# Optimization experiments

Measured on AMD Instinct MI355X. Metric: run time of the kernel, lower is better.

Reference implementation:

```python
import jax, jax.numpy as jnp
from jax import lax
import numpy as np

T_STEPS, C_IN, H_IN, W_IN = 15, 6, 256, 256
C_OUT, KSIZE = 64, 5
THRESH = 15.0   # conv_t[0]
KWTA = 5        # ks[0]
INH_R = 3       # inh_radiuses[0]


def setup_inputs() -> dict:
    key = jax.random.key(0)
    k1, k2 = jax.random.split(key)
    # cumulative binary spike-wave: once a unit spikes it stays on (SpykeTorch convention)
    bern = jax.random.uniform(k1, (T_STEPS, C_IN, H_IN, W_IN)) < 0.05
    spikes = (jnp.cumsum(bern.astype(jnp.int32), axis=0) > 0).astype(jnp.float32)
    # SpykeTorch Convolution init: N(0.8, 0.05)
    w1 = 0.8 + 0.05 * jax.random.normal(k2, (C_OUT, C_IN, KSIZE, KSIZE), dtype=jnp.float32)
    return {"input": spikes, "w1": w1, "current_layer_id": 1}


def pointwise_inhibition(thr_pot):
    # thr_pot: (T, C, H, W). Keep, at each spatial position, only the feature
    # with the earliest spike (ties broken by max potential); zero the rest.
    T = thr_pot.shape[0]
    C = thr_pot.shape[1]
    max_vals = jnp.max(thr_pot, axis=1, keepdims=True)            # (T,1,H,W)
    max_idx = jnp.argmax(thr_pot, axis=1, keepdims=True)          # (T,1,H,W)
    clamp_pot = jnp.sign(max_vals)                                # (T,1,H,W) in {0,1}
    earliest = jnp.clip((T - clamp_pot.sum(axis=0, keepdims=True)).astype(jnp.int32), 0, T - 1)  # (1,1,H,W)
    winners = jnp.take_along_axis(max_idx, earliest, axis=0)      # (1,1,H,W)
    onehot = (jnp.arange(C)[None, :, None, None] == winners[:, 0])  # (1,C,H,W)
    coef = onehot.astype(thr_pot.dtype) * clamp_pot[-1:]          # zero where no spike at last step
    return thr_pot * coef


def get_k_winners(pot, spk, kwta, inh_radius):
    # pot, spk: (T, C, H, W). Returns (kwta, 3) int winners (c, h, w); -1 rows = no winner.
    T, C, H, W = pot.shape
    earliest = jnp.clip((T - spk.sum(axis=0, keepdims=True)).astype(jnp.int32), 0, T - 1)
    values = jnp.take_along_axis(pot, earliest, axis=0)           # (1,C,H,W)
    trunc = spk * values
    v = trunc.max() * T
    trunc = trunc + spk * v
    total = trunc.sum(axis=0)                                     # (C,H,W)
    rows = jnp.arange(H)
    cols = jnp.arange(W)

    def step(total, _):
        idx = jnp.argmax(total)
        val = total.reshape(-1)[idx]
        c = idx // (H * W)
        rem = idx % (H * W)
        h = rem // W
        w = rem % W
        winner = jnp.where(val != 0,
                           jnp.stack([c, h, w]),
                           jnp.full((3,), -1, dtype=idx.dtype))
        total = total.at[c].set(0.0)
        box = (((rows >= h - inh_radius) & (rows <= h + inh_radius))[:, None]
               & ((cols >= w - inh_radius) & (cols <= w + inh_radius))[None, :])
        total = jnp.where(box[None, :, :], 0.0, total)            # columnar spatial inhibition
        return total, winner

    _, winners = lax.scan(step, total, None, length=kwta)
    return winners


def reference(input, w1, current_layer_id):
    # training path, current_layer_id == 1
    x = jnp.pad(input.astype(jnp.float32), ((0, 0), (0, 0), (2, 2), (2, 2)))  # sf.pad (2,2,2,2)
    pot = lax.conv_general_dilated(x, w1, (1, 1), 'VALID',
                                   dimension_numbers=('NCHW', 'OIHW', 'NCHW'))  # (T,64,256,256)
    pot = jnp.where(pot < THRESH, 0.0, pot)   # sf.fire -> thresholded potentials
    pot = pointwise_inhibition(pot)
    spk = jnp.sign(pot)
    winners = get_k_winners(pot, spk, KWTA, INH_R)
    return spk, pot, winners
```

## Files before the change

### kernel.cpp

```cpp
#include <hip/hip_runtime.h>
#include <hip/hip_cooperative_groups.h>
#include <stdint.h>

namespace cg = cooperative_groups;

static constexpr int T_STEPS = 15;
static constexpr int C_IN = 6;
static constexpr int C_OUT = 64;
static constexpr int H = 256;
static constexpr int W = 256;
static constexpr int NPOS = H * W;
static constexpr int NTAP = 150;
#define DTHRESH 15.0

typedef float vfloat4 __attribute__((ext_vector_type(4)));

static constexpr size_t WS_FT     = 0;
static constexpr size_t WS_SERIES = 393216;
static constexpr size_t WS_WINC   = WS_SERIES + (size_t)NPOS*16*4;
static constexpr size_t WS_NMAP   = WS_WINC + (size_t)NPOS;
static constexpr size_t WS_VAL    = WS_NMAP + (size_t)NPOS;
static constexpr size_t WS_RED    = WS_VAL + (size_t)NPOS*8;
static constexpr size_t WS_RIX    = WS_RED + 128*8;
static constexpr size_t WS_NEED   = WS_RIX + 128*4;

__global__ __launch_bounds__(256) void ft_kernel(const float* __restrict__ x,
                                                 uint8_t* __restrict__ ft) {
    int i = blockIdx.x * 256 + threadIdx.x;
    if (i >= C_IN * NPOS) return;
    int f = 15;
    #pragma unroll
    for (int t = T_STEPS - 1; t >= 0; --t) {
        if (x[(size_t)t * (C_IN * NPOS) + i] > 0.0f) f = t;
    }
    ft[i] = (uint8_t)f;
}

__global__ __launch_bounds__(256, 4) void conv_kernel(
        const float* __restrict__ w1, const uint8_t* __restrict__ ftg,
        float* __restrict__ series_ws, int8_t* __restrict__ winc_ws,
        uint8_t* __restrict__ nmap_ws, double* __restrict__ val_ws)
{
    __shared__ float w_lds[(NTAP + 1) * 64];
    __shared__ uint8_t ft_lds[6 * 5 * 20];
    __shared__ alignas(16) unsigned cnt_lds[4][16];
    __shared__ alignas(8) uint8_t sorted_lds[4][200];

    int tid = threadIdx.x;
    int bid = blockIdx.x;
    int h  = bid >> 4;
    int w0 = (bid & 15) << 4;

    for (int i = tid; i < C_OUT * NTAP; i += 256) {
        int o = i / NTAP;
        int tap = i - o * NTAP;
        w_lds[tap * 64 + o] = w1[i];
    }
    if (tid < 64) w_lds[NTAP * 64 + tid] = 0.0f;
    for (int i = tid; i < 600; i += 256) {
        int c = i / 100;
        int r = i - c * 100;
        int kh = r / 20;
        int j  = r - kh * 20;
        int gh = h - 2 + kh;
        int gw = w0 - 2 + j;
        uint8_t v = 15;
        if (gh >= 0 && gh < H && gw >= 0 && gw < W) v = ftg[c * NPOS + gh * W + gw];
        ft_lds[(c * 5 + kh) * 20 + j] = v;
    }
    __syncthreads();

    int lane = tid & 63;
    int wvi  = tid >> 6;
    unsigned* cnt = cnt_lds[wvi];
    uint8_t* srt = sorted_lds[wvi];

    for (int iter = 0; iter < 4; ++iter) {
        int xl = iter * 4 + wvi;
        int p  = h * W + w0 + xl;

        if (lane < 16) cnt[lane] = 0;

        int tap0 = lane, tap1 = lane + 64, tap2 = lane + 128;
        auto ftv = [&](int tap) -> unsigned {
            int c = tap / 25;
            int r = tap - c * 25;
            int kh = r / 5;
            int kw = r - kh * 5;
            return ft_lds[(c * 5 + kh) * 20 + xl + kw];
        };
        unsigned f0 = ftv(tap0);
        unsigned f1 = ftv(tap1);
        unsigned f2 = (tap2 < NTAP) ? ftv(tap2) : 15u;
        unsigned r0 = 0, r1 = 0, r2 = 0;
        if (f0 < 15u) r0 = atomicAdd(&cnt[f0], 1u);
        if (f1 < 15u) r1 = atomicAdd(&cnt[f1], 1u);
        if (f2 < 15u) r2 = atomicAdd(&cnt[f2], 1u);

        uint4 c4[4];
        #pragma unroll
        for (int i = 0; i < 4; ++i) c4[i] = ((const uint4*)cnt)[i];
        unsigned cv_t[16];
        #pragma unroll
        for (int i = 0; i < 4; ++i) {
            cv_t[4*i+0] = c4[i].x; cv_t[4*i+1] = c4[i].y;
            cv_t[4*i+2] = c4[i].z; cv_t[4*i+3] = c4[i].w;
        }
        int kt[15];
        #pragma unroll
        for (int t = 0; t < 15; ++t) kt[t] = (int)__builtin_amdgcn_readfirstlane(cv_t[t]);

        unsigned st0 = 0, st1 = 0, st2 = 0, stp = 0;
        #pragma unroll
        for (int t = 0; t < 15; ++t) {
            unsigned a = (cv_t[t] + 3u) & ~3u;
            if ((unsigned)t < f0) st0 += a;
            if ((unsigned)t < f1) st1 += a;
            if ((unsigned)t < f2) st2 += a;
            if (t < lane) stp += a;
        }
        if (f0 < 15u) srt[st0 + r0] = (uint8_t)tap0;
        if (f1 < 15u) srt[st1 + r1] = (uint8_t)tap1;
        if (f2 < 15u) srt[st2 + r2] = (uint8_t)tap2;

        if (lane < 15) {
            unsigned kk = cnt[lane];
            unsigned a4 = (kk + 3u) & ~3u;
            if (kk     < a4) srt[stp + kk]     = (uint8_t)NTAP;
            if (kk + 1 < a4) srt[stp + kk + 1] = (uint8_t)NTAP;
            if (kk + 2 < a4) srt[stp + kk + 2] = (uint8_t)NTAP;
        }

        double run = 0.0, cvv = 0.0;
        int tc = 127;
        float ser[15];
        int A = 0;
        #pragma unroll
        for (int t = 0; t < 15; ++t) {
            int k = kt[t];
            for (int q = 0; q < k; q += 4) {
                unsigned pr = *(const unsigned*)(srt + A + q);
                float wa  = w_lds[((pr       & 0xFFu) << 6) + lane];
                float wb  = w_lds[(((pr >> 8) & 0xFFu) << 6) + lane];
                float wcf = w_lds[(((pr >> 16) & 0xFFu) << 6) + lane];
                float wd  = w_lds[(( pr >> 24        ) << 6) + lane];
                float s   = (wa + wb) + (wcf + wd);
                run += (double)s;
            }
            A += (k + 3) & ~3;
            ser[t] = (float)run;
            bool cross_now = (tc == 127) && (run >= DTHRESH);
            if (cross_now) { tc = t; cvv = run; }
        }

        int e = tc;
        #pragma unroll
        for (int off = 32; off >= 1; off >>= 1) e = min(e, __shfl_xor(e, off));
        int wc = -1;
        double val = 0.0;
        if (e < 15) {
            double vl = (tc == e) ? cvv : 0.0;
            double m = vl;
            #pragma unroll
            for (int off = 32; off >= 1; off >>= 1) m = fmax(m, __shfl_xor(m, off));
            unsigned long long mk = __ballot(vl == m);
            wc = __ffsll(mk) - 1;
            val = m;

            float ov = 0.0f;
            #pragma unroll
            for (int t = 0; t < 15; ++t) {
                float sv = __shfl(ser[t], wc);
                if (lane == t) ov = sv;
            }
            if (lane < e) ov = 0.0f;
            if (lane < 15) series_ws[p * 16 + lane] = ov;
        }
        if (lane == 0) {
            winc_ws[p] = (int8_t)wc;
            nmap_ws[p] = (uint8_t)(wc >= 0 ? (15 - e) : 0);
            if (wc >= 0) val_ws[p] = val;
        }
    }
}

__global__ __launch_bounds__(256) void kwin_kernel(
        const int8_t* __restrict__ winc, const uint8_t* __restrict__ nmap,
        const double* __restrict__ val, float* __restrict__ outw,
        double* __restrict__ redv, unsigned* __restrict__ redi)
{
    cg::grid_group grid = cg::this_grid();
    const int tid  = threadIdx.x;
    const int bid  = blockIdx.x;
    const int lane = tid & 63, wvi = tid >> 6;

    __shared__ double   s_v[4];
    __shared__ unsigned s_i[4];

    int     pc[4];
    int     phh[4], pww[4];
    double  key[4];
    unsigned idx[4];
    bool    alive[4];
    #pragma unroll
    for (int k = 0; k < 4; ++k) {
        const int p = (k << 14) | (bid << 8) | tid;
        const int c = winc[p];
        alive[k] = (c >= 0);
        const double vp = alive[k] ? val[p] : 0.0;
        key[k]  = (double)nmap[p] * 2048.0 + vp;
        idx[k]  = ((unsigned)c << 16) | (unsigned)p;
        pc[k]   = c;
        phh[k]  = p >> 8;
        pww[k]  = p & 255;
    }

    for (int r = 0; r < 5; ++r) {
        __syncthreads();
        const int par = r & 1;

        double   bv = -1.0;
        unsigned bi = 0xFFFFFFFFu;
        #pragma unroll
        for (int k = 0; k < 4; ++k) {
            if (alive[k] && (key[k] > bv || (key[k] == bv && idx[k] < bi))) {
                bv = key[k]; bi = idx[k];
            }
        }
        #pragma unroll
        for (int off = 32; off >= 1; off >>= 1) {
            double   ov = __shfl_xor(bv, off);
            unsigned oi = __shfl_xor(bi, off);
            if (ov > bv || (ov == bv && oi < bi)) { bv = ov; bi = oi; }
        }
        if (lane == 0) { s_v[wvi] = bv; s_i[wvi] = bi; }
        __syncthreads();
        if (tid == 0) {
            double bbv = s_v[0]; unsigned bbi = s_i[0];
            #pragma unroll
            for (int i = 1; i < 4; ++i)
                if (s_v[i] > bbv || (s_v[i] == bbv && s_i[i] < bbi)) { bbv = s_v[i]; bbi = s_i[i]; }
            redv[par * 64 + bid] = bbv;
            redi[par * 64 + bid] = bbi;
        }
        grid.sync();

        if (wvi == 0) {
            double   gv = redv[par * 64 + lane];
            unsigned gi = redi[par * 64 + lane];
            #pragma unroll
            for (int off = 32; off >= 1; off >>= 1) {
                double   ov = __shfl_xor(gv, off);
                unsigned oi = __shfl_xor(gi, off);
                if (ov > gv || (ov == gv && oi < gi)) { gv = ov; gi = oi; }
            }
            if (lane == 0) { s_v[0] = gv; s_i[0] = gi; }
        }
        __syncthreads();
        const double   bbv = s_v[0];
        const unsigned bbi = s_i[0];

        const bool valid = (bbv > 0.0);
        if (bid == 0 && tid == 0) {
            int wc2 = (int)(bbi >> 16), pp = (int)(bbi & 0xFFFFu);
            outw[r * 3 + 0] = valid ? (float)wc2       : -1.0f;
            outw[r * 3 + 1] = valid ? (float)(pp >> 8) : -1.0f;
            outw[r * 3 + 2] = valid ? (float)(pp & 255): -1.0f;
        }
        if (valid) {
            const int wc2 = (int)(bbi >> 16);
            const int wp  = (int)(bbi & 0xFFFFu);
            const int wh  = wp >> 8, wwv = wp & 255;
            #pragma unroll
            for (int k = 0; k < 4; ++k) {
                if (pc[k] == wc2 || (phh[k] >= wh - 3 && phh[k] <= wh + 3 &&
                                     pww[k] >= wwv - 3 && pww[k] <= wwv + 3)) alive[k] = false;
            }
        }
    }
}

__global__ __launch_bounds__(256) void expand_kernel(
        const int8_t* __restrict__ winc, const float* __restrict__ series,
        float* __restrict__ spk, float* __restrict__ pot)
{
    int idx4 = blockIdx.x * 256 + threadIdx.x;
    int w4 = idx4 & 63;
    int h  = (idx4 >> 6) & 255;
    int c  = (idx4 >> 14) & 63;
    int t  = idx4 >> 20;
    int pbase = h * W + (w4 << 2);
    uint32_t wcs = *reinterpret_cast<const uint32_t*>(winc + pbase);
    vfloat4 pv = (vfloat4)(0.0f);
    vfloat4 sv = (vfloat4)(0.0f);
    #pragma unroll
    for (int e2 = 0; e2 < 4; ++e2) {
        int8_t wcb = (int8_t)((wcs >> (8 * e2)) & 0xFFu);
        if ((int)wcb == c) {
            float xv = series[(size_t)(pbase + e2) * 16 + t];
            pv[e2] = xv;
            sv[e2] = (xv > 0.f) ? 1.0f : 0.0f;
        }
    }
    reinterpret_cast<vfloat4*>(spk)[idx4] = sv;
    reinterpret_cast<vfloat4*>(pot)[idx4] = pv;
}

extern "C" void kernel_launch(void* const* d_in, const int* in_sizes, int n_in,
                              void* d_out, int out_size, void* d_ws, size_t ws_size,
                              hipStream_t stream)
{
    if (ws_size < WS_NEED) return;

    const float* x  = (const float*)d_in[0];
    const float* w1 = (const float*)d_in[1];
    uint8_t* ws = (uint8_t*)d_ws;
    uint8_t* ftg    = ws + WS_FT;
    float*   series = (float*)(ws + WS_SERIES);
    int8_t*  winc   = (int8_t*)(ws + WS_WINC);
    uint8_t* nmap   = (uint8_t*)(ws + WS_NMAP);
    double*  val    = (double*)(ws + WS_VAL);
    double*  redv   = (double*)(ws + WS_RED);
    unsigned* redi  = (unsigned*)(ws + WS_RIX);

    float* spk  = (float*)d_out;
    float* pot  = spk + (size_t)T_STEPS * C_OUT * NPOS;
    float* outw = pot + (size_t)T_STEPS * C_OUT * NPOS;

    hipLaunchKernelGGL(ft_kernel,     dim3(1536),  dim3(256),  0, stream, x, ftg);
    hipLaunchKernelGGL(conv_kernel,   dim3(4096),  dim3(256),  0, stream, w1, ftg, series, winc, nmap, val);

    void* kargs[] = { (void*)&winc, (void*)&nmap, (void*)&val,
                      (void*)&outw, (void*)&redv, (void*)&redi };
    hipLaunchCooperativeKernel((const void*)kwin_kernel, dim3(64), dim3(256), kargs, 0, stream);

    hipLaunchKernelGGL(expand_kernel, dim3(61440), dim3(256),  0, stream, winc, series, spk, pot);
}
```

Before: 752.2 us.

## Fuse k-winners selection with output expansion in one cooperative kernel

Merges the k-winners cooperative kernel and the spike/potential expansion kernel into one cooperative launch of 1024 blocks. The first 256 blocks each own one position for the winner reduction. All blocks write a slice of the large spk/pot outputs between grid syncs, so the output stores overlap the serial reduction rounds. The final cross-block reduce now spans 256 partials. The cost is that every block must stay co-resident for grid.sync, and the stores now share time with the synchronisation.

New measurement: 1.432 ms. 90.3% more time.

```diff
diff --git a/kernel.cpp b/kernel.cpp
--- a/kernel.cpp
+++ b/kernel.cpp
@@ -21,8 +21,8 @@
 static constexpr size_t WS_NMAP   = WS_WINC + (size_t)NPOS;
 static constexpr size_t WS_VAL    = WS_NMAP + (size_t)NPOS;
 static constexpr size_t WS_RED    = WS_VAL + (size_t)NPOS*8;
-static constexpr size_t WS_RIX    = WS_RED + 128*8;
-static constexpr size_t WS_NEED   = WS_RIX + 128*4;
+static constexpr size_t WS_RIX    = WS_RED + 512*8;
+static constexpr size_t WS_NEED   = WS_RIX + 512*4;
 
 __global__ __launch_bounds__(256) void ft_kernel(const float* __restrict__ x,
                                                  uint8_t* __restrict__ ft) {
@@ -184,49 +184,42 @@
     }
 }
 
-__global__ __launch_bounds__(256) void kwin_kernel(
+__global__ __launch_bounds__(256, 8) void kwin_expand_kernel(
         const int8_t* __restrict__ winc, const uint8_t* __restrict__ nmap,
-        const double* __restrict__ val, float* __restrict__ outw,
+        const double* __restrict__ val, const float* __restrict__ series,
+        float* __restrict__ outw, float* __restrict__ spk, float* __restrict__ pot,
         double* __restrict__ redv, unsigned* __restrict__ redi)
 {
     cg::grid_group grid = cg::this_grid();
     const int tid  = threadIdx.x;
     const int bid  = blockIdx.x;
+    const int gid  = (bid << 8) | tid;
     const int lane = tid & 63, wvi = tid >> 6;
 
     __shared__ double   s_v[4];
     __shared__ unsigned s_i[4];
 
-    int     pc[4];
-    int     phh[4], pww[4];
-    double  key[4];
-    unsigned idx[4];
-    bool    alive[4];
-    #pragma unroll
-    for (int k = 0; k < 4; ++k) {
-        const int p = (k << 14) | (bid << 8) | tid;
+    const bool own = (bid < 256);
+    int     pc = -1, phh = -99, pww = -99;
+    double  key = -1.0;
+    unsigned idx = 0xFFFFFFFFu;
+    bool    alive = false;
+    if (own) {
+        const int p = gid;
         const int c = winc[p];
-        alive[k] = (c >= 0);
-        const double vp = alive[k] ? val[p] : 0.0;
-        key[k]  = (double)nmap[p] * 2048.0 + vp;
-        idx[k]  = ((unsigned)c << 16) | (unsigned)p;
-        pc[k]   = c;
-        phh[k]  = p >> 8;
-        pww[k]  = p & 255;
+        alive = (c >= 0);
+        const double vp = alive ? val[p] : 0.0;
+        key = (double)nmap[p] * 2048.0 + vp;
+        idx = ((unsigned)c << 16) | (unsigned)p;
+        pc = c; phh = p >> 8; pww = p & 255;
     }
 
     for (int r = 0; r < 5; ++r) {
         __syncthreads();
         const int par = r & 1;
 
-        double   bv = -1.0;
-        unsigned bi = 0xFFFFFFFFu;
-        #pragma unroll
-        for (int k = 0; k < 4; ++k) {
-            if (alive[k] && (key[k] > bv || (key[k] == bv && idx[k] < bi))) {
-                bv = key[k]; bi = idx[k];
-            }
-        }
+        double   bv = alive ? key : -1.0;
+        unsigned bi = alive ? idx : 0xFFFFFFFFu;
         #pragma unroll
         for (int off = 32; off >= 1; off >>= 1) {
             double   ov = __shfl_xor(bv, off);
@@ -235,30 +228,55 @@
         }
         if (lane == 0) { s_v[wvi] = bv; s_i[wvi] = bi; }
         __syncthreads();
-        if (tid == 0) {
+        if (own && tid == 0) {
             double bbv = s_v[0]; unsigned bbi = s_i[0];
             #pragma unroll
             for (int i = 1; i < 4; ++i)
                 if (s_v[i] > bbv || (s_v[i] == bbv && s_i[i] < bbi)) { bbv = s_v[i]; bbi = s_i[i]; }
-            redv[par * 64 + bid] = bbv;
-            redi[par * 64 + bid] = bbi;
-        }
+            redv[par * 256 + bid] = bbv;
+            redi[par * 256 + bid] = bbi;
+        }
+
+        #pragma unroll
+        for (int j = 0; j < 12; ++j) {
+            int idx4 = (r * 12 + j) * 262144 + gid;
+            int w4 = idx4 & 63;
+            int h  = (idx4 >> 6) & 255;
+            int c  = (idx4 >> 14) & 63;
+            int t  = idx4 >> 20;
+            int pbase = h * W + (w4 << 2);
+            uint32_t wcs = *reinterpret_cast<const uint32_t*>(winc + pbase);
+            vfloat4 pv = (vfloat4)(0.0f);
+            vfloat4 sv = (vfloat4)(0.0f);
+            #pragma unroll
+            for (int e2 = 0; e2 < 4; ++e2) {
+                int8_t wcb = (int8_t)((wcs >> (8 * e2)) & 0xFFu);
+                if ((int)wcb == c) {
+                    float xv = series[(size_t)(pbase + e2) * 16 + t];
+                    pv[e2] = xv;
+                    sv[e2] = (xv > 0.f) ? 1.0f : 0.0f;
+                }
+            }
+            reinterpret_cast<vfloat4*>(spk)[idx4] = sv;
+            reinterpret_cast<vfloat4*>(pot)[idx4] = pv;
+        }
+
         grid.sync();
 
-        if (wvi == 0) {
-            double   gv = redv[par * 64 + lane];
-            unsigned gi = redi[par * 64 + lane];
-            #pragma unroll
-            for (int off = 32; off >= 1; off >>= 1) {
-                double   ov = __shfl_xor(gv, off);
-                unsigned oi = __shfl_xor(gi, off);
-                if (ov > gv || (ov == gv && oi < gi)) { gv = ov; gi = oi; }
-            }
-            if (lane == 0) { s_v[0] = gv; s_i[0] = gi; }
-        }
+        double   gv = redv[par * 256 + tid];
+        unsigned gi = redi[par * 256 + tid];
+        #pragma unroll
+        for (int off = 32; off >= 1; off >>= 1) {
+            double   ov = __shfl_xor(gv, off);
+            unsigned oi = __shfl_xor(gi, off);
+            if (ov > gv || (ov == gv && oi < gi)) { gv = ov; gi = oi; }
+        }
+        if (lane == 0) { s_v[wvi] = gv; s_i[wvi] = gi; }
         __syncthreads();
-        const double   bbv = s_v[0];
-        const unsigned bbi = s_i[0];
+        double bbv = s_v[0]; unsigned bbi = s_i[0];
+        #pragma unroll
+        for (int i = 1; i < 4; ++i)
+            if (s_v[i] > bbv || (s_v[i] == bbv && s_i[i] < bbi)) { bbv = s_v[i]; bbi = s_i[i]; }
 
         const bool valid = (bbv > 0.0);
         if (bid == 0 && tid == 0) {
@@ -267,43 +285,14 @@
             outw[r * 3 + 1] = valid ? (float)(pp >> 8) : -1.0f;
             outw[r * 3 + 2] = valid ? (float)(pp & 255): -1.0f;
         }
-        if (valid) {
+        if (valid && own) {
             const int wc2 = (int)(bbi >> 16);
             const int wp  = (int)(bbi & 0xFFFFu);
             const int wh  = wp >> 8, wwv = wp & 255;
-            #pragma unroll
-            for (int k = 0; k < 4; ++k) {
-                if (pc[k] == wc2 || (phh[k] >= wh - 3 && phh[k] <= wh + 3 &&
-                                     pww[k] >= wwv - 3 && pww[k] <= wwv + 3)) alive[k] = false;
-            }
-        }
-    }
-}
-
-__global__ __launch_bounds__(256) void expand_kernel(
-        const int8_t* __restrict__ winc, const float* __restrict__ series,
-        float* __restrict__ spk, float* __restrict__ pot)
-{
-    int idx4 = blockIdx.x * 256 + threadIdx.x;
-    int w4 = idx4 & 63;
-    int h  = (idx4 >> 6) & 255;
-    int c  = (idx4 >> 14) & 63;
-    int t  = idx4 >> 20;
-    int pbase = h * W + (w4 << 2);
-    uint32_t wcs = *reinterpret_cast<const uint32_t*>(winc + pbase);
-    vfloat4 pv = (vfloat4)(0.0f);
-    vfloat4 sv = (vfloat4)(0.0f);
-    #pragma unroll
-    for (int e2 = 0; e2 < 4; ++e2) {
-        int8_t wcb = (int8_t)((wcs >> (8 * e2)) & 0xFFu);
-        if ((int)wcb == c) {
-            float xv = series[(size_t)(pbase + e2) * 16 + t];
-            pv[e2] = xv;
-            sv[e2] = (xv > 0.f) ? 1.0f : 0.0f;
-        }
-    }
-    reinterpret_cast<vfloat4*>(spk)[idx4] = sv;
-    reinterpret_cast<vfloat4*>(pot)[idx4] = pv;
+            if (pc == wc2 || (phh >= wh - 3 && phh <= wh + 3 &&
+                              pww >= wwv - 3 && pww <= wwv + 3)) alive = false;
+        }
+    }
 }
 
 extern "C" void kernel_launch(void* const* d_in, const int* in_sizes, int n_in,
@@ -330,9 +319,8 @@
     hipLaunchKernelGGL(ft_kernel,     dim3(1536),  dim3(256),  0, stream, x, ftg);
     hipLaunchKernelGGL(conv_kernel,   dim3(4096),  dim3(256),  0, stream, w1, ftg, series, winc, nmap, val);
 
-    void* kargs[] = { (void*)&winc, (void*)&nmap, (void*)&val,
-                      (void*)&outw, (void*)&redv, (void*)&redi };
-    hipLaunchCooperativeKernel((const void*)kwin_kernel, dim3(64), dim3(256), kargs, 0, stream);
-
-    hipLaunchKernelGGL(expand_kernel, dim3(61440), dim3(256),  0, stream, winc, series, spk, pot);
+    void* kargs[] = { (void*)&winc, (void*)&nmap, (void*)&val, (void*)&series,
+                      (void*)&outw, (void*)&spk, (void*)&pot,
+                      (void*)&redv, (void*)&redi };
+    hipLaunchCooperativeKernel((const void*)kwin_expand_kernel, dim3(1024), dim3(256), kargs, 0, stream);
 }
```

## Replace dense expand with memset plus sparse scatter; restructure conv blocks

Applied to the files above, without the earlier changes.

The output-expansion kernel, which computed and wrote every (t,c,h,w) element, is replaced by a hipMemsetAsync that zeroes the spk/pot outputs and a small scatter kernel. The scatter writes only the 15 time steps of each position's single winning channel. The conv kernel now uses 512-thread blocks with one position per wave instead of looping over four positions per wave, and prefetches the next sorted tap word. Memset bandwidth should beat the compute-and-write path, but the scattered writes are strided by NPOS and poorly coalesced, and the larger blocks with a persistent weight table in LDS may reduce occupancy.

Result: slower. 861.6 us (+14.5%).

```diff
diff --git a/kernel.cpp b/kernel.cpp
--- a/kernel.cpp
+++ b/kernel.cpp
@@ -36,37 +36,37 @@
     ft[i] = (uint8_t)f;
 }
 
-__global__ __launch_bounds__(256, 4) void conv_kernel(
+__global__ __launch_bounds__(512, 6) void conv_kernel(
         const float* __restrict__ w1, const uint8_t* __restrict__ ftg,
         float* __restrict__ series_ws, int8_t* __restrict__ winc_ws,
         uint8_t* __restrict__ nmap_ws, double* __restrict__ val_ws)
 {
     __shared__ float w_lds[(NTAP + 1) * 64];
-    __shared__ uint8_t ft_lds[6 * 5 * 20];
-    __shared__ alignas(16) unsigned cnt_lds[4][16];
-    __shared__ alignas(8) uint8_t sorted_lds[4][200];
+    __shared__ uint8_t ft_lds[6 * 5 * 12];
+    __shared__ alignas(16) unsigned cnt_lds[8][16];
+    __shared__ alignas(8) uint8_t sorted_lds[8][204];
 
     int tid = threadIdx.x;
     int bid = blockIdx.x;
-    int h  = bid >> 4;
-    int w0 = (bid & 15) << 4;
-
-    for (int i = tid; i < C_OUT * NTAP; i += 256) {
+    int h  = bid >> 5;
+    int w0 = (bid & 31) << 3;
+
+    for (int i = tid; i < C_OUT * NTAP; i += 512) {
         int o = i / NTAP;
         int tap = i - o * NTAP;
         w_lds[tap * 64 + o] = w1[i];
     }
     if (tid < 64) w_lds[NTAP * 64 + tid] = 0.0f;
-    for (int i = tid; i < 600; i += 256) {
-        int c = i / 100;
-        int r = i - c * 100;
-        int kh = r / 20;
-        int j  = r - kh * 20;
+    for (int i = tid; i < 360; i += 512) {
+        int c = i / 60;
+        int r = i - c * 60;
+        int kh = r / 12;
+        int j  = r - kh * 12;
         int gh = h - 2 + kh;
         int gw = w0 - 2 + j;
         uint8_t v = 15;
         if (gh >= 0 && gh < H && gw >= 0 && gw < W) v = ftg[c * NPOS + gh * W + gw];
-        ft_lds[(c * 5 + kh) * 20 + j] = v;
+        ft_lds[(c * 5 + kh) * 12 + j] = v;
     }
     __syncthreads();
 
@@ -75,112 +75,112 @@
     unsigned* cnt = cnt_lds[wvi];
     uint8_t* srt = sorted_lds[wvi];
 
-    for (int iter = 0; iter < 4; ++iter) {
-        int xl = iter * 4 + wvi;
-        int p  = h * W + w0 + xl;
-
-        if (lane < 16) cnt[lane] = 0;
-
-        int tap0 = lane, tap1 = lane + 64, tap2 = lane + 128;
-        auto ftv = [&](int tap) -> unsigned {
-            int c = tap / 25;
-            int r = tap - c * 25;
-            int kh = r / 5;
-            int kw = r - kh * 5;
-            return ft_lds[(c * 5 + kh) * 20 + xl + kw];
-        };
-        unsigned f0 = ftv(tap0);
-        unsigned f1 = ftv(tap1);
-        unsigned f2 = (tap2 < NTAP) ? ftv(tap2) : 15u;
-        unsigned r0 = 0, r1 = 0, r2 = 0;
-        if (f0 < 15u) r0 = atomicAdd(&cnt[f0], 1u);
-        if (f1 < 15u) r1 = atomicAdd(&cnt[f1], 1u);
-        if (f2 < 15u) r2 = atomicAdd(&cnt[f2], 1u);
-
-        uint4 c4[4];
+    int xl = wvi;
+    int p  = h * W + w0 + xl;
+
+    if (lane < 16) cnt[lane] = 0;
+
+    int tap0 = lane, tap1 = lane + 64, tap2 = lane + 128;
+    auto ftv = [&](int tap) -> unsigned {
+        int c = tap / 25;
+        int r = tap - c * 25;
+        int kh = r / 5;
+        int kw = r - kh * 5;
+        return ft_lds[(c * 5 + kh) * 12 + xl + kw];
+    };
+    unsigned f0 = ftv(tap0);
+    unsigned f1 = ftv(tap1);
+    unsigned f2 = (tap2 < NTAP) ? ftv(tap2) : 15u;
+    unsigned r0 = 0, r1 = 0, r2 = 0;
+    if (f0 < 15u) r0 = atomicAdd(&cnt[f0], 1u);
+    if (f1 < 15u) r1 = atomicAdd(&cnt[f1], 1u);
+    if (f2 < 15u) r2 = atomicAdd(&cnt[f2], 1u);
+
+    uint4 c4[4];
+    #pragma unroll
+    for (int i = 0; i < 4; ++i) c4[i] = ((const uint4*)cnt)[i];
+    unsigned cv_t[16];
+    #pragma unroll
+    for (int i = 0; i < 4; ++i) {
+        cv_t[4*i+0] = c4[i].x; cv_t[4*i+1] = c4[i].y;
+        cv_t[4*i+2] = c4[i].z; cv_t[4*i+3] = c4[i].w;
+    }
+    int kt[15];
+    #pragma unroll
+    for (int t = 0; t < 15; ++t) kt[t] = (int)__builtin_amdgcn_readfirstlane(cv_t[t]);
+
+    unsigned st0 = 0, st1 = 0, st2 = 0, stp = 0;
+    #pragma unroll
+    for (int t = 0; t < 15; ++t) {
+        unsigned a = (cv_t[t] + 3u) & ~3u;
+        if ((unsigned)t < f0) st0 += a;
+        if ((unsigned)t < f1) st1 += a;
+        if ((unsigned)t < f2) st2 += a;
+        if (t < lane) stp += a;
+    }
+    if (f0 < 15u) srt[st0 + r0] = (uint8_t)tap0;
+    if (f1 < 15u) srt[st1 + r1] = (uint8_t)tap1;
+    if (f2 < 15u) srt[st2 + r2] = (uint8_t)tap2;
+
+    if (lane < 15) {
+        unsigned kk = cnt[lane];
+        unsigned a4 = (kk + 3u) & ~3u;
+        if (kk     < a4) srt[stp + kk]     = (uint8_t)NTAP;
+        if (kk + 1 < a4) srt[stp + kk + 1] = (uint8_t)NTAP;
+        if (kk + 2 < a4) srt[stp + kk + 2] = (uint8_t)NTAP;
+    }
+
+    double run = 0.0, cvv = 0.0;
+    int tc = 127;
+    float ser[15];
+    int A = 0;
+    unsigned pr = *(const unsigned*)(srt);
+    #pragma unroll
+    for (int t = 0; t < 15; ++t) {
+        int k = kt[t];
+        for (int q = 0; q < k; q += 4) {
+            unsigned nxt = *(const unsigned*)(srt + A + q + 4);
+            float wa  = w_lds[((pr       & 0xFFu) << 6) + lane];
+            float wb  = w_lds[(((pr >> 8) & 0xFFu) << 6) + lane];
+            float wcf = w_lds[(((pr >> 16) & 0xFFu) << 6) + lane];
+            float wd  = w_lds[(( pr >> 24        ) << 6) + lane];
+            float s   = (wa + wb) + (wcf + wd);
+            run += (double)s;
+            pr = nxt;
+        }
+        A += (k + 3) & ~3;
+        ser[t] = (float)run;
+        bool cross_now = (tc == 127) && (run >= DTHRESH);
+        if (cross_now) { tc = t; cvv = run; }
+    }
+
+    int e = tc;
+    #pragma unroll
+    for (int off = 32; off >= 1; off >>= 1) e = min(e, __shfl_xor(e, off));
+    int wc = -1;
+    double val = 0.0;
+    if (e < 15) {
+        double vl = (tc == e) ? cvv : 0.0;
+        double m = vl;
         #pragma unroll
-        for (int i = 0; i < 4; ++i) c4[i] = ((const uint4*)cnt)[i];
-        unsigned cv_t[16];
-        #pragma unroll
-        for (int i = 0; i < 4; ++i) {
-            cv_t[4*i+0] = c4[i].x; cv_t[4*i+1] = c4[i].y;
-            cv_t[4*i+2] = c4[i].z; cv_t[4*i+3] = c4[i].w;
-        }
-        int kt[15];
-        #pragma unroll
-        for (int t = 0; t < 15; ++t) kt[t] = (int)__builtin_amdgcn_readfirstlane(cv_t[t]);
-
-        unsigned st0 = 0, st1 = 0, st2 = 0, stp = 0;
+        for (int off = 32; off >= 1; off >>= 1) m = fmax(m, __shfl_xor(m, off));
+        unsigned long long mk = __ballot(vl == m);
+        wc = __ffsll(mk) - 1;
+        val = m;
+
+        float ov = 0.0f;
         #pragma unroll
         for (int t = 0; t < 15; ++t) {
-            unsigned a = (cv_t[t] + 3u) & ~3u;
-            if ((unsigned)t < f0) st0 += a;
-            if ((unsigned)t < f1) st1 += a;
-            if ((unsigned)t < f2) st2 += a;
-            if (t < lane) stp += a;
-        }
-        if (f0 < 15u) srt[st0 + r0] = (uint8_t)tap0;
-        if (f1 < 15u) srt[st1 + r1] = (uint8_t)tap1;
-        if (f2 < 15u) srt[st2 + r2] = (uint8_t)tap2;
-
-        if (lane < 15) {
-            unsigned kk = cnt[lane];
-            unsigned a4 = (kk + 3u) & ~3u;
-            if (kk     < a4) srt[stp + kk]     = (uint8_t)NTAP;
-            if (kk + 1 < a4) srt[stp + kk + 1] = (uint8_t)NTAP;
-            if (kk + 2 < a4) srt[stp + kk + 2] = (uint8_t)NTAP;
-        }
-
-        double run = 0.0, cvv = 0.0;
-        int tc = 127;
-        float ser[15];
-        int A = 0;
-        #pragma unroll
-        for (int t = 0; t < 15; ++t) {
-            int k = kt[t];
-            for (int q = 0; q < k; q += 4) {
-                unsigned pr = *(const unsigned*)(srt + A + q);
-                float wa  = w_lds[((pr       & 0xFFu) << 6) + lane];
-                float wb  = w_lds[(((pr >> 8) & 0xFFu) << 6) + lane];
-                float wcf = w_lds[(((pr >> 16) & 0xFFu) << 6) + lane];
-                float wd  = w_lds[(( pr >> 24        ) << 6) + lane];
-                float s   = (wa + wb) + (wcf + wd);
-                run += (double)s;
-            }
-            A += (k + 3) & ~3;
-            ser[t] = (float)run;
-            bool cross_now = (tc == 127) && (run >= DTHRESH);
-            if (cross_now) { tc = t; cvv = run; }
-        }
-
-        int e = tc;
-        #pragma unroll
-        for (int off = 32; off >= 1; off >>= 1) e = min(e, __shfl_xor(e, off));
-        int wc = -1;
-        double val = 0.0;
-        if (e < 15) {
-            double vl = (tc == e) ? cvv : 0.0;
-            double m = vl;
-            #pragma unroll
-            for (int off = 32; off >= 1; off >>= 1) m = fmax(m, __shfl_xor(m, off));
-            unsigned long long mk = __ballot(vl == m);
-            wc = __ffsll(mk) - 1;
-            val = m;
-
-            float ov = 0.0f;
-            #pragma unroll
-            for (int t = 0; t < 15; ++t) {
-                float sv = __shfl(ser[t], wc);
-                if (lane == t) ov = sv;
-            }
-            if (lane < e) ov = 0.0f;
-            if (lane < 15) series_ws[p * 16 + lane] = ov;
-        }
-        if (lane == 0) {
-            winc_ws[p] = (int8_t)wc;
-            nmap_ws[p] = (uint8_t)(wc >= 0 ? (15 - e) : 0);
-            if (wc >= 0) val_ws[p] = val;
-        }
+            float sv = __shfl(ser[t], wc);
+            if (lane == t) ov = sv;
+        }
+        if (lane < e) ov = 0.0f;
+        if (lane < 15) series_ws[p * 16 + lane] = ov;
+    }
+    if (lane == 0) {
+        winc_ws[p] = (int8_t)wc;
+        nmap_ws[p] = (uint8_t)(wc >= 0 ? (15 - e) : 0);
+        if (wc >= 0) val_ws[p] = val;
     }
 }
 
@@ -280,30 +280,25 @@
     }
 }
 
-__global__ __launch_bounds__(256) void expand_kernel(
+__global__ __launch_bounds__(256) void scatter_kernel(
         const int8_t* __restrict__ winc, const float* __restrict__ series,
         float* __restrict__ spk, float* __restrict__ pot)
 {
-    int idx4 = blockIdx.x * 256 + threadIdx.x;
-    int w4 = idx4 & 63;
-    int h  = (idx4 >> 6) & 255;
-    int c  = (idx4 >> 14) & 63;
-    int t  = idx4 >> 20;
-    int pbase = h * W + (w4 << 2);
-    uint32_t wcs = *reinterpret_cast<const uint32_t*>(winc + pbase);
-    vfloat4 pv = (vfloat4)(0.0f);
-    vfloat4 sv = (vfloat4)(0.0f);
-    #pragma unroll
-    for (int e2 = 0; e2 < 4; ++e2) {
-        int8_t wcb = (int8_t)((wcs >> (8 * e2)) & 0xFFu);
-        if ((int)wcb == c) {
-            float xv = series[(size_t)(pbase + e2) * 16 + t];
-            pv[e2] = xv;
-            sv[e2] = (xv > 0.f) ? 1.0f : 0.0f;
-        }
-    }
-    reinterpret_cast<vfloat4*>(spk)[idx4] = sv;
-    reinterpret_cast<vfloat4*>(pot)[idx4] = pv;
+    int p = blockIdx.x * 256 + threadIdx.x;
+    int c = winc[p];
+    if (c < 0) return;
+    const vfloat4* sp = reinterpret_cast<const vfloat4*>(series + (size_t)p * 16);
+    vfloat4 q0 = sp[0], q1 = sp[1], q2 = sp[2], q3 = sp[3];
+    float sv[16];
+    #pragma unroll
+    for (int j = 0; j < 4; ++j) { sv[j] = q0[j]; sv[4+j] = q1[j]; sv[8+j] = q2[j]; sv[12+j] = q3[j]; }
+    size_t base = (size_t)c * NPOS + (size_t)p;
+    #pragma unroll
+    for (int t = 0; t < 15; ++t) {
+        float xv = sv[t];
+        pot[(size_t)t * (C_OUT * NPOS) + base] = xv;
+        spk[(size_t)t * (C_OUT * NPOS) + base] = (xv > 0.f) ? 1.0f : 0.0f;
+    }
 }
 
 extern "C" void kernel_launch(void* const* d_in, const int* in_sizes, int n_in,
@@ -327,12 +322,14 @@
     float* pot  = spk + (size_t)T_STEPS * C_OUT * NPOS;
     float* outw = pot + (size_t)T_STEPS * C_OUT * NPOS;
 
+    hipMemsetAsync(d_out, 0, (size_t)2 * T_STEPS * C_OUT * NPOS * sizeof(float), stream);
+
     hipLaunchKernelGGL(ft_kernel,     dim3(1536),  dim3(256),  0, stream, x, ftg);
-    hipLaunchKernelGGL(conv_kernel,   dim3(4096),  dim3(256),  0, stream, w1, ftg, series, winc, nmap, val);
+    hipLaunchKernelGGL(conv_kernel,   dim3(8192),  dim3(512),  0, stream, w1, ftg, series, winc, nmap, val);
 
     void* kargs[] = { (void*)&winc, (void*)&nmap, (void*)&val,
                       (void*)&outw, (void*)&redv, (void*)&redi };
     hipLaunchCooperativeKernel((const void*)kwin_kernel, dim3(64), dim3(256), kargs, 0, stream);
 
-    hipLaunchKernelGGL(expand_kernel, dim3(61440), dim3(256),  0, stream, winc, series, spk, pot);
-}
+    hipLaunchKernelGGL(scatter_kernel, dim3(256),  dim3(256),  0, stream, winc, series, spk, pot);
+}
```
